# Performance work log

Hardware: AMD Instinct MI355X
Metric: run time of the kernel (lower is better)

The kernel has to match this reference:

```python
import jax, jax.numpy as jnp
import numpy as np
from jax import lax

BN_EPS = 1e-5


def _spatial_gate(x, w, g, b, m, v):
    # x: [N, C, H, W]; ChannelPool -> [N, 2, H, W]; 7x7 conv -> [N,1,H,W]; BN (eval); sigmoid gate
    comp = jnp.stack([jnp.max(x, axis=1), jnp.mean(x, axis=1)], axis=1)
    o = lax.conv_general_dilated(comp, w, (1, 1), [(3, 3), (3, 3)],
                                 dimension_numbers=('NCHW', 'OIHW', 'NCHW'))
    o = (o - m[None, :, None, None]) * lax.rsqrt(v + BN_EPS)[None, :, None, None] \
        * g[None, :, None, None] + b[None, :, None, None]
    s = jax.nn.sigmoid(o)
    return x * s


def _eca_sort(x, w_eca):
    # global avg pool -> sort channels desc -> 1D conv over sorted seq -> sigmoid -> unsort -> gate
    y = jnp.mean(x, axis=(2, 3))               # [N, C]
    order = jnp.argsort(-y, axis=1)            # descending sort indices
    rank = jnp.argsort(order, axis=1)          # inverse permutation
    ys = jnp.take_along_axis(y, order, axis=1)  # sorted descending
    k = w_eca.shape[-1]
    p = k // 2
    o = lax.conv_general_dilated(ys[:, None, :], w_eca, (1,), [(p, p)],
                                 dimension_numbers=('NCH', 'OIH', 'NCH'))[:, 0, :]
    sig = jax.nn.sigmoid(o)
    yr = jnp.take_along_axis(sig, rank, axis=1)  # reorder back per original index_select(rank)
    return x * yr[:, :, None, None]


def setup_inputs() -> dict:
    key = jax.random.key(0)
    ks = jax.random.split(key, 6)
    N, C, H, W = 32, 256, 56, 56
    inp = {
        'x': jax.random.normal(ks[0], (N, C, H, W), dtype=jnp.float32),
        'weight': jax.random.normal(ks[1], (1,), dtype=jnp.float32),
        'w_h': jax.random.normal(ks[2], (1, 2, 7, 7), dtype=jnp.float32) * 0.1,
        'g_h': jnp.ones((1,), jnp.float32), 'b_h': jnp.zeros((1,), jnp.float32),
        'm_h': jnp.zeros((1,), jnp.float32), 'v_h': jnp.ones((1,), jnp.float32),
        'w_w': jax.random.normal(ks[3], (1, 2, 7, 7), dtype=jnp.float32) * 0.1,
        'g_w': jnp.ones((1,), jnp.float32), 'b_w': jnp.zeros((1,), jnp.float32),
        'm_w': jnp.zeros((1,), jnp.float32), 'v_w': jnp.ones((1,), jnp.float32),
        'w_s': jax.random.normal(ks[4], (1, 2, 7, 7), dtype=jnp.float32) * 0.1,
        'g_s': jnp.ones((1,), jnp.float32), 'b_s': jnp.zeros((1,), jnp.float32),
        'm_s': jnp.zeros((1,), jnp.float32), 'v_s': jnp.ones((1,), jnp.float32),
        'w_eca': jax.random.normal(ks[5], (1, 1, 5), dtype=jnp.float32) * 0.3,
    }
    return inp


def reference(x, weight, w_h, g_h, b_h, m_h, v_h, w_w, g_w, b_w, m_w, v_w,
              w_s, g_s, b_s, m_s, v_s, w_eca):
    # branch 1: gate over H-as-channel (permute 0,2,1,3)
    xh = jnp.transpose(x, (0, 2, 1, 3))
    x11 = jnp.transpose(_spatial_gate(xh, w_h, g_h, b_h, m_h, v_h), (0, 2, 1, 3))
    # branch 2: gate over W-as-channel (permute 0,3,2,1)
    xw = jnp.transpose(x, (0, 3, 2, 1))
    x21 = jnp.transpose(_spatial_gate(xw, w_w, g_w, b_w, m_w, v_w), (0, 3, 2, 1))
    # branch 3: eca with sort/unsort
    x31 = _eca_sort(x, w_eca)
    # branch 4: plain spatial gate
    xo = _spatial_gate(x, w_s, g_s, b_s, m_s, v_s)
    return 0.23779 * xo + 0.24695 * x11 + 0.24365 * x21 + 0.27173 * x31
```

## Files before the change

### kernel.cpp

```cpp
#include <hip/hip_runtime.h>
#include <math.h>

#define N_ 32
#define C_ 256
#define H_ 56
#define W_ 56
#define HW_ (H_*W_)
#define HW4_ (HW_/4)
#define CHW_ (C_*HW_)
#define NHW_ (N_*HW_)
#define NHW4_ (NHW_/4)
#define NCW_ (N_*C_*W_)
#define NHC_ (N_*H_*C_)
#define BN_EPS_ 1e-5f

#define TLD 60
#define PLANES_PER_BLK 8
#define NB_PL 1024

#define SM_BUF1 3360
#define SM_CPMX 6720
#define SM_CPSM (6720 + 224)
#define SM_TOT  (6720 + 448)

#define F4MAX(a,b) do { (a).x=fmaxf((a).x,(b).x); (a).y=fmaxf((a).y,(b).y); \
                        (a).z=fmaxf((a).z,(b).z); (a).w=fmaxf((a).w,(b).w); } while(0)
#define F4ADD(a,b) do { (a).x+=(b).x; (a).y+=(b).y; (a).z+=(b).z; (a).w+=(b).w; } while(0)

__global__ __launch_bounds__(256, 4) void pools_k(
        const float* __restrict__ x,
        float* __restrict__ maxH, float* __restrict__ meanH,
        float* __restrict__ maxWt, float* __restrict__ meanWt,
        float* __restrict__ pmx, float* __restrict__ psm,
        float* __restrict__ y) {
    __shared__ float smem[SM_TOT];
    int b = blockIdx.x;
    int tid = threadIdx.x;
    const float4* x4 = (const float4*)x;
    float* buf0 = smem;
    float* buf1 = smem + SM_BUF1;
    float* cpmx = smem + SM_CPMX;
    float* cpsm = smem + SM_CPSM;
    int pb0 = b * PLANES_PER_BLK;
    float4 r0, r1, r2, r3;
    int row0 = tid / 14,          col0 = (tid % 14) * 4;
    int row1 = (tid + 256) / 14,  col1 = ((tid + 256) % 14) * 4;
    int row2 = (tid + 512) / 14,  col2 = ((tid + 512) % 14) * 4;
    int row3 = (tid + 768) / 14,  col3 = ((tid + 768) % 14) * 4;
    float4 amx0, amx1, amx2, amx3, asm0, asm1, asm2, asm3;
    amx0 = amx1 = amx2 = amx3 = make_float4(-INFINITY, -INFINITY, -INFINITY, -INFINITY);
    asm0 = asm1 = asm2 = asm3 = make_float4(0.f, 0.f, 0.f, 0.f);
    {
        size_t base = (size_t)pb0 * HW4_;
        r0 = x4[base + tid];
        r1 = x4[base + 256 + tid];
        r2 = x4[base + 512 + tid];
        if (tid < 16) r3 = x4[base + 768 + tid];
        F4MAX(amx0, r0); F4ADD(asm0, r0);
        F4MAX(amx1, r1); F4ADD(asm1, r1);
        F4MAX(amx2, r2); F4ADD(asm2, r2);
        if (tid < 16) { F4MAX(amx3, r3); F4ADD(asm3, r3); }
        *(float4*)&buf0[row0 * TLD + col0] = r0;
        *(float4*)&buf0[row1 * TLD + col1] = r1;
        *(float4*)&buf0[row2 * TLD + col2] = r2;
        if (tid < 16) *(float4*)&buf0[row3 * TLD + col3] = r3;
    }
    __syncthreads();
    for (int k = 0; k < PLANES_PER_BLK; ++k) {
        float* cur = (k & 1) ? buf1 : buf0;
        float* nxt = (k & 1) ? buf0 : buf1;
        int pb = pb0 + k;
        int n = pb >> 8, c = pb & 255;
        if (k < PLANES_PER_BLK - 1) {
            size_t base = (size_t)(pb + 1) * HW4_;
            r0 = x4[base + tid];
            r1 = x4[base + 256 + tid];
            r2 = x4[base + 512 + tid];
            if (tid < 16) r3 = x4[base + 768 + tid];
        }
        if (tid < 224) {
            int w = tid % 56, hq = tid / 56;
            const float* base = &cur[(hq * 14) * TLD + w];
            float mx = -INFINITY, sm = 0.f;
            #pragma unroll
            for (int hh = 0; hh < 14; ++hh) {
                float v = base[hh * TLD];
                mx = fmaxf(mx, v); sm += v;
            }
            cpmx[hq * 56 + w] = mx;
            cpsm[hq * 56 + w] = sm;
        }
        if (tid < 224) {
            int h = tid >> 2, kq = tid & 3;
            const float* base = &cur[h * TLD + kq * 14];
            float mx = -INFINITY, sm = 0.f;
            #pragma unroll
            for (int kk = 0; kk < 14; ++kk) {
                float v = base[kk];
                mx = fmaxf(mx, v); sm += v;
            }
            mx = fmaxf(mx, __shfl_xor(mx, 1)); sm += __shfl_xor(sm, 1);
            mx = fmaxf(mx, __shfl_xor(mx, 2)); sm += __shfl_xor(sm, 2);
            if (kq == 0) {
                int o = (n * C_ + c) * H_ + h;
                maxWt[o] = mx;
                meanWt[o] = sm * (1.f / W_);
            }
        }
        __syncthreads();
        float colsum = 0.f;
        if (tid < 56) {
            float mx = cpmx[tid], sm = cpsm[tid];
            #pragma unroll
            for (int j = 1; j < 4; ++j) {
                mx = fmaxf(mx, cpmx[j * 56 + tid]);
                sm += cpsm[j * 56 + tid];
            }
            int o = (n * C_ + c) * W_ + tid;
            maxH[o] = mx;
            meanH[o] = sm * (1.f / H_);
            colsum = sm;
        }
        if (tid < 64) {
            float t = colsum;
            #pragma unroll
            for (int off = 32; off >= 1; off >>= 1) t += __shfl_xor(t, off);
            if (tid == 0) y[n * C_ + c] = t * (1.f / HW_);
        }
        if (k < PLANES_PER_BLK - 1) {
            F4MAX(amx0, r0); F4ADD(asm0, r0);
            F4MAX(amx1, r1); F4ADD(asm1, r1);
            F4MAX(amx2, r2); F4ADD(asm2, r2);
            if (tid < 16) { F4MAX(amx3, r3); F4ADD(asm3, r3); }
            *(float4*)&nxt[row0 * TLD + col0] = r0;
            *(float4*)&nxt[row1 * TLD + col1] = r1;
            *(float4*)&nxt[row2 * TLD + col2] = r2;
            if (tid < 16) *(float4*)&nxt[row3 * TLD + col3] = r3;
        }
        __syncthreads();
    }
    {
        float4* PM = (float4*)pmx + (size_t)b * HW4_;
        float4* PS = (float4*)psm + (size_t)b * HW4_;
        PM[tid] = amx0;        PS[tid] = asm0;
        PM[tid + 256] = amx1;  PS[tid + 256] = asm1;
        PM[tid + 512] = amx2;  PS[tid + 512] = asm2;
        if (tid < 16) { PM[tid + 768] = amx3; PS[tid + 768] = asm3; }
    }
}

__global__ __launch_bounds__(256, 4) void cpool_final_k(
        const float* __restrict__ pmx, const float* __restrict__ psm,
        float* __restrict__ maxC, float* __restrict__ meanC) {
    __shared__ float4 smx[4][64];
    __shared__ float4 ssm[4][64];
    int bb = blockIdx.x;
    int tid = threadIdx.x;
    int oi = tid & 63, g4 = tid >> 6;
    int t = bb * 64 + oi;
    int n = t / HW4_, hw4 = t - n * HW4_;
    const float4* PM = (const float4*)pmx + (size_t)(n * 32 + g4 * 8) * HW4_ + hw4;
    const float4* PS = (const float4*)psm + (size_t)(n * 32 + g4 * 8) * HW4_ + hw4;
    float4 mx = make_float4(-INFINITY, -INFINITY, -INFINITY, -INFINITY);
    float4 sm = make_float4(0.f, 0.f, 0.f, 0.f);
    #pragma unroll
    for (int g = 0; g < 8; ++g) {
        float4 v = PM[(size_t)g * HW4_];
        float4 s = PS[(size_t)g * HW4_];
        F4MAX(mx, v);
        F4ADD(sm, s);
    }
    smx[g4][oi] = mx;
    ssm[g4][oi] = sm;
    __syncthreads();
    if (tid < 64) {
        float4 m = smx[0][tid];
        #pragma unroll
        for (int j = 1; j < 4; ++j) {
            float4 v = smx[j][tid];
            F4MAX(m, v);
        }
        ((float4*)maxC)[bb * 64 + tid] = m;
    } else if (tid < 128) {
        int t2 = tid - 64;
        float4 s = ssm[0][t2];
        #pragma unroll
        for (int j = 1; j < 4; ++j) {
            float4 v = ssm[j][t2];
            F4ADD(s, v);
        }
        s.x *= (1.f / C_); s.y *= (1.f / C_); s.z *= (1.f / C_); s.w *= (1.f / C_);
        ((float4*)meanC)[bb * 64 + t2] = s;
    }
}

template <int R, int Cc, bool TR>
__device__ __forceinline__ void conv7_part(int t, const float* __restrict__ p0,
                                           const float* __restrict__ p1,
                                           const float* __restrict__ wt,
                                           float g, float bb, float m, float v,
                                           float* __restrict__ out) {
    const int per = R * Cc;
    int n = t / per;
    int r2 = t - n * per;
    int i = r2 / Cc, j = r2 - i * Cc;
    const float* b0 = p0 + (size_t)n * per;
    const float* b1 = p1 + (size_t)n * per;
    float acc = 0.f;
    #pragma unroll
    for (int ki = 0; ki < 7; ++ki) {
        int ii = i + ki - 3;
        if (ii < 0 || ii >= R) continue;
        #pragma unroll
        for (int kj = 0; kj < 7; ++kj) {
            int jj = j + kj - 3;
            if (jj < 0 || jj >= Cc) continue;
            int idx = ii * Cc + jj;
            int wi = TR ? (kj * 7 + ki) : (ki * 7 + kj);
            acc += b0[idx] * wt[wi] + b1[idx] * wt[49 + wi];
        }
    }
    float o = (acc - m) * rsqrtf(v + BN_EPS_) * g + bb;
    out[t] = 1.f / (1.f + expf(-o));
}

#define NB_SS (NHW_ / 256)
#define NB_SH (NCW_ / 256)
#define NB_SW (NHC_ / 256)

__global__ __launch_bounds__(256) void conv_eca_k(
        const float* __restrict__ maxC, const float* __restrict__ meanC,
        const float* __restrict__ maxH, const float* __restrict__ meanH,
        const float* __restrict__ maxWt, const float* __restrict__ meanWt,
        const float* __restrict__ w_s, const float* __restrict__ g_s,
        const float* __restrict__ b_s, const float* __restrict__ m_s,
        const float* __restrict__ v_s,
        const float* __restrict__ w_h, const float* __restrict__ g_h,
        const float* __restrict__ b_h, const float* __restrict__ m_h,
        const float* __restrict__ v_h,
        const float* __restrict__ w_w, const float* __restrict__ g_w,
        const float* __restrict__ b_w, const float* __restrict__ m_w,
        const float* __restrict__ v_w,
        const float* __restrict__ y, const float* __restrict__ w_eca,
        float* __restrict__ s_s, float* __restrict__ s_h, float* __restrict__ s_wt,
        float* __restrict__ gate) {
    __shared__ float sv[C_];
    __shared__ int si[C_];
    int b = blockIdx.x;
    int tid = threadIdx.x;
    if (b < NB_SS) {
        conv7_part<H_, W_, false>(b * 256 + tid, maxC, meanC, w_s, g_s[0], b_s[0],
                                  m_s[0], v_s[0], s_s);
    } else if (b < NB_SS + NB_SH) {
        conv7_part<C_, W_, false>((b - NB_SS) * 256 + tid, maxH, meanH, w_h, g_h[0],
                                  b_h[0], m_h[0], v_h[0], s_h);
    } else if (b < NB_SS + NB_SH + NB_SW) {
        conv7_part<C_, H_, true>((b - NB_SS - NB_SH) * 256 + tid, maxWt, meanWt, w_w,
                                 g_w[0], b_w[0], m_w[0], v_w[0], s_wt);
    } else {
        int n = b - (NB_SS + NB_SH + NB_SW);
        sv[tid] = y[n * C_ + tid];
        si[tid] = tid;
        __syncthreads();
        for (int k = 2; k <= C_; k <<= 1) {
            for (int j = k >> 1; j > 0; j >>= 1) {
                int ixj = tid ^ j;
                if (ixj > tid) {
                    float v1 = sv[tid], v2 = sv[ixj];
                    int i1 = si[tid], i2 = si[ixj];
                    bool before = (v1 > v2) || (v1 == v2 && i1 < i2);
                    bool dir = ((tid & k) == 0);
                    if (dir ? !before : before) {
                        sv[tid] = v2; sv[ixj] = v1;
                        si[tid] = i2; si[ixj] = i1;
                    }
                }
                __syncthreads();
            }
        }
        float o = 0.f;
        #pragma unroll
        for (int j = 0; j < 5; ++j) {
            int p = tid + j - 2;
            if (p >= 0 && p < C_) o += sv[p] * w_eca[j];
        }
        gate[n * C_ + si[tid]] = 1.f / (1.f + expf(-o));
    }
}

__global__ __launch_bounds__(256) void apply_k(
        const float* __restrict__ x, const float* __restrict__ s_s,
        const float* __restrict__ s_h, const float* __restrict__ s_wt,
        const float* __restrict__ gate, float* __restrict__ out) {
    int t0 = blockIdx.x * 512 + threadIdx.x;
    #pragma unroll
    for (int r = 0; r < 2; ++r) {
        int t = t0 + r * 256;
        int f = t * 4;
        int n = f / CHW_;
        int rem = f - n * CHW_;
        int c = rem / HW_;
        int hw = rem - c * HW_;
        int h = hw / W_;
        int w = hw - h * W_;
        float4 xv = ((const float4*)x)[t];
        float4 s4 = *(const float4*)(s_s + (size_t)n * HW_ + hw);
        float4 h4 = *(const float4*)(s_h + ((size_t)n * C_ + c) * W_ + w);
        float sw = s_wt[((size_t)n * C_ + c) * H_ + h];
        float ge = gate[n * C_ + c];
        float base = 0.24365f * sw + 0.27173f * ge;
        float4 o;
        o.x = xv.x * (0.23779f * s4.x + 0.24695f * h4.x + base);
        o.y = xv.y * (0.23779f * s4.y + 0.24695f * h4.y + base);
        o.z = xv.z * (0.23779f * s4.z + 0.24695f * h4.z + base);
        o.w = xv.w * (0.23779f * s4.w + 0.24695f * h4.w + base);
        ((float4*)out)[t] = o;
    }
}

extern "C" void kernel_launch(void* const* d_in, const int* in_sizes, int n_in,
                              void* d_out, int out_size, void* d_ws, size_t ws_size,
                              hipStream_t stream) {
    const float* x     = (const float*)d_in[0];
    const float* w_h   = (const float*)d_in[2];
    const float* g_h   = (const float*)d_in[3];
    const float* b_h   = (const float*)d_in[4];
    const float* m_h   = (const float*)d_in[5];
    const float* v_h   = (const float*)d_in[6];
    const float* w_w   = (const float*)d_in[7];
    const float* g_w   = (const float*)d_in[8];
    const float* b_w   = (const float*)d_in[9];
    const float* m_w   = (const float*)d_in[10];
    const float* v_w   = (const float*)d_in[11];
    const float* w_s   = (const float*)d_in[12];
    const float* g_s   = (const float*)d_in[13];
    const float* b_s   = (const float*)d_in[14];
    const float* m_s   = (const float*)d_in[15];
    const float* v_s   = (const float*)d_in[16];
    const float* w_eca = (const float*)d_in[17];
    float* out = (float*)d_out;

    float* ws    = (float*)d_ws;
    float* maxC  = ws;
    float* meanC = maxC  + NHW_;
    float* maxH  = meanC + NHW_;
    float* meanH = maxH  + NCW_;
    float* maxWt = meanH + NCW_;
    float* meanWt= maxWt + NHC_;
    float* s_s   = meanWt+ NHC_;
    float* s_h   = s_s   + NHW_;
    float* s_wt  = s_h   + NCW_;
    float* yv    = s_wt  + NHC_;
    float* gate  = yv    + N_ * C_;
    float* pmx   = gate  + N_ * C_;
    float* psm   = pmx   + (size_t)NB_PL * HW_;

    pools_k<<<NB_PL, 256, 0, stream>>>(x, maxH, meanH, maxWt, meanWt, pmx, psm, yv);

    cpool_final_k<<<NHW4_ / 64, 256, 0, stream>>>(pmx, psm, maxC, meanC);

    int conv_blocks = NB_SS + NB_SH + NB_SW + N_;
    conv_eca_k<<<conv_blocks, 256, 0, stream>>>(maxC, meanC, maxH, meanH, maxWt, meanWt,
                                                w_s, g_s, b_s, m_s, v_s,
                                                w_h, g_h, b_h, m_h, v_h,
                                                w_w, g_w, b_w, m_w, v_w,
                                                yv, w_eca, s_s, s_h, s_wt, gate);

    apply_k<<<(N_ * CHW_ / 4) / 512, 256, 0, stream>>>(x, s_s, s_h, s_wt, gate, out);
}
```

Before: 93.70 us.

## Deepen pools kernel prefetch to two planes with triple-buffered LDS

The pooling kernel now processes 16 planes per block instead of 8 and keeps two planes of global loads in flight using two register sets and three LDS tile buffers. The loop is unrolled by two so one plane's loads are issued while the previous plane is reduced. This aims to hide more global memory latency and to halve the partial channel-pool buffers that the final reduction kernel reads. In exchange it uses more registers and shared memory per block and launches half as many blocks, which may lower occupancy and parallelism.

```diff
diff --git a/kernel.cpp b/kernel.cpp
--- a/kernel.cpp
+++ b/kernel.cpp
@@ -15,13 +15,13 @@
 #define BN_EPS_ 1e-5f
 
 #define TLD 60
-#define PLANES_PER_BLK 8
-#define NB_PL 1024
-
-#define SM_BUF1 3360
-#define SM_CPMX 6720
-#define SM_CPSM (6720 + 224)
-#define SM_TOT  (6720 + 448)
+#define PPB 16
+#define NB_PL 512
+
+#define SM_B(i) ((i) * 3360)
+#define SM_CPMX 10080
+#define SM_CPSM (10080 + 224)
+#define SM_TOT  (10080 + 448)
 
 #define F4MAX(a,b) do { (a).x=fmaxf((a).x,(b).x); (a).y=fmaxf((a).y,(b).y); \
                         (a).z=fmaxf((a).z,(b).z); (a).w=fmaxf((a).w,(b).w); } while(0)
@@ -37,108 +37,108 @@
     int b = blockIdx.x;
     int tid = threadIdx.x;
     const float4* x4 = (const float4*)x;
-    float* buf0 = smem;
-    float* buf1 = smem + SM_BUF1;
     float* cpmx = smem + SM_CPMX;
     float* cpsm = smem + SM_CPSM;
-    int pb0 = b * PLANES_PER_BLK;
-    float4 r0, r1, r2, r3;
+    int pb0 = b * PPB;
     int row0 = tid / 14,          col0 = (tid % 14) * 4;
     int row1 = (tid + 256) / 14,  col1 = ((tid + 256) % 14) * 4;
     int row2 = (tid + 512) / 14,  col2 = ((tid + 512) % 14) * 4;
     int row3 = (tid + 768) / 14,  col3 = ((tid + 768) % 14) * 4;
+    float4 a0, a1, a2, a3;
+    float4 b0_, b1_, b2_, b3_;
     float4 amx0, amx1, amx2, amx3, asm0, asm1, asm2, asm3;
     amx0 = amx1 = amx2 = amx3 = make_float4(-INFINITY, -INFINITY, -INFINITY, -INFINITY);
     asm0 = asm1 = asm2 = asm3 = make_float4(0.f, 0.f, 0.f, 0.f);
-    {
-        size_t base = (size_t)pb0 * HW4_;
-        r0 = x4[base + tid];
-        r1 = x4[base + 256 + tid];
-        r2 = x4[base + 512 + tid];
-        if (tid < 16) r3 = x4[base + 768 + tid];
-        F4MAX(amx0, r0); F4ADD(asm0, r0);
-        F4MAX(amx1, r1); F4ADD(asm1, r1);
-        F4MAX(amx2, r2); F4ADD(asm2, r2);
-        if (tid < 16) { F4MAX(amx3, r3); F4ADD(asm3, r3); }
-        *(float4*)&buf0[row0 * TLD + col0] = r0;
-        *(float4*)&buf0[row1 * TLD + col1] = r1;
-        *(float4*)&buf0[row2 * TLD + col2] = r2;
-        if (tid < 16) *(float4*)&buf0[row3 * TLD + col3] = r3;
-    }
+
+#define ISSUE(R0,R1,R2,R3, P) { size_t _ba = (size_t)(pb0 + (P)) * HW4_;          \
+        R0 = x4[_ba + tid]; R1 = x4[_ba + 256 + tid]; R2 = x4[_ba + 512 + tid];   \
+        if (tid < 16) R3 = x4[_ba + 768 + tid]; }
+#define FOLD(R0,R1,R2,R3) { F4MAX(amx0,R0); F4ADD(asm0,R0);                       \
+        F4MAX(amx1,R1); F4ADD(asm1,R1); F4MAX(amx2,R2); F4ADD(asm2,R2);           \
+        if (tid < 16) { F4MAX(amx3,R3); F4ADD(asm3,R3); } }
+#define STAGE(BUF, R0,R1,R2,R3) { float* _d = smem + (BUF);                       \
+        *(float4*)&_d[row0*TLD+col0] = R0; *(float4*)&_d[row1*TLD+col1] = R1;     \
+        *(float4*)&_d[row2*TLD+col2] = R2;                                        \
+        if (tid < 16) *(float4*)&_d[row3*TLD+col3] = R3; }
+
+    ISSUE(a0, a1, a2, a3, 0);
+    FOLD(a0, a1, a2, a3);
+    STAGE(SM_B(0), a0, a1, a2, a3);
+    ISSUE(b0_, b1_, b2_, b3_, 1);
     __syncthreads();
-    for (int k = 0; k < PLANES_PER_BLK; ++k) {
-        float* cur = (k & 1) ? buf1 : buf0;
-        float* nxt = (k & 1) ? buf0 : buf1;
-        int pb = pb0 + k;
-        int n = pb >> 8, c = pb & 255;
-        if (k < PLANES_PER_BLK - 1) {
-            size_t base = (size_t)(pb + 1) * HW4_;
-            r0 = x4[base + tid];
-            r1 = x4[base + 256 + tid];
-            r2 = x4[base + 512 + tid];
-            if (tid < 16) r3 = x4[base + 768 + tid];
-        }
-        if (tid < 224) {
-            int w = tid % 56, hq = tid / 56;
-            const float* base = &cur[(hq * 14) * TLD + w];
-            float mx = -INFINITY, sm = 0.f;
-            #pragma unroll
-            for (int hh = 0; hh < 14; ++hh) {
-                float v = base[hh * TLD];
-                mx = fmaxf(mx, v); sm += v;
-            }
-            cpmx[hq * 56 + w] = mx;
-            cpsm[hq * 56 + w] = sm;
-        }
-        if (tid < 224) {
-            int h = tid >> 2, kq = tid & 3;
-            const float* base = &cur[h * TLD + kq * 14];
-            float mx = -INFINITY, sm = 0.f;
-            #pragma unroll
-            for (int kk = 0; kk < 14; ++kk) {
-                float v = base[kk];
-                mx = fmaxf(mx, v); sm += v;
-            }
-            mx = fmaxf(mx, __shfl_xor(mx, 1)); sm += __shfl_xor(sm, 1);
-            mx = fmaxf(mx, __shfl_xor(mx, 2)); sm += __shfl_xor(sm, 2);
-            if (kq == 0) {
-                int o = (n * C_ + c) * H_ + h;
-                maxWt[o] = mx;
-                meanWt[o] = sm * (1.f / W_);
-            }
+
+#define COMPUTE(K) {                                                              \
+        const float* cur = smem + SM_B((K) % 3);                                  \
+        int pb = pb0 + (K);                                                       \
+        int n = pb >> 8, c = pb & 255;                                            \
+        if (tid < 224) {                     \
+            int w = tid % 56, hq = tid / 56;                                      \
+            const float* base = &cur[(hq * 14) * TLD + w];                        \
+            float mx = -INFINITY, sm = 0.f;                                       \
+            _Pragma("unroll")                                                     \
+            for (int hh = 0; hh < 14; ++hh) {                                     \
+                float v = base[hh * TLD];                                         \
+                mx = fmaxf(mx, v); sm += v;                                       \
+            }                                                                     \
+            cpmx[hq * 56 + w] = mx; cpsm[hq * 56 + w] = sm;                       \
+        }                                                                         \
+        if (tid < 224) {                     \
+            int h = tid >> 2, kq = tid & 3;                                       \
+            const float* base = &cur[h * TLD + kq * 14];                          \
+            float mx = -INFINITY, sm = 0.f;                                       \
+            _Pragma("unroll")                                                     \
+            for (int kk = 0; kk < 14; ++kk) {                                     \
+                float v = base[kk];                                               \
+                mx = fmaxf(mx, v); sm += v;                                       \
+            }                                                                     \
+            mx = fmaxf(mx, __shfl_xor(mx, 1)); sm += __shfl_xor(sm, 1);           \
+            mx = fmaxf(mx, __shfl_xor(mx, 2)); sm += __shfl_xor(sm, 2);           \
+            if (kq == 0) {                                                        \
+                int o = (n * C_ + c) * H_ + h;                                    \
+                maxWt[o] = mx; meanWt[o] = sm * (1.f / W_);                       \
+            }                                                                     \
+        }                                                                         \
+        __syncthreads();                                                          \
+        float colsum = 0.f;                                                       \
+        if (tid < 56) {                                                           \
+            float mx = cpmx[tid], sm = cpsm[tid];                                 \
+            _Pragma("unroll")                                                     \
+            for (int j = 1; j < 4; ++j) {                                         \
+                mx = fmaxf(mx, cpmx[j * 56 + tid]);                               \
+                sm += cpsm[j * 56 + tid];                                         \
+            }                                                                     \
+            int o = (n * C_ + c) * W_ + tid;                                      \
+            maxH[o] = mx; meanH[o] = sm * (1.f / H_);                             \
+            colsum = sm;                                                          \
+        }                                                                         \
+        if (tid < 64) {                                                           \
+            float t = colsum;                                                     \
+            _Pragma("unroll")                                                     \
+            for (int off = 32; off >= 1; off >>= 1) t += __shfl_xor(t, off);      \
+            if (tid == 0) y[n * C_ + c] = t * (1.f / HW_);                        \
+        }                                                                         \
+    }
+
+    #pragma unroll
+    for (int k2 = 0; k2 < PPB / 2; ++k2) {
+        const int k = 2 * k2;
+        if (k + 2 < PPB) ISSUE(a0, a1, a2, a3, k + 2);
+        COMPUTE(k);
+        FOLD(b0_, b1_, b2_, b3_);
+        STAGE(SM_B((k + 1) % 3), b0_, b1_, b2_, b3_);
+        __syncthreads();
+        if (k + 3 < PPB) ISSUE(b0_, b1_, b2_, b3_, k + 3);
+        COMPUTE(k + 1);
+        if (k + 2 < PPB) {
+            FOLD(a0, a1, a2, a3);
+            STAGE(SM_B((k + 2) % 3), a0, a1, a2, a3);
         }
         __syncthreads();
-        float colsum = 0.f;
-        if (tid < 56) {
-            float mx = cpmx[tid], sm = cpsm[tid];
-            #pragma unroll
-            for (int j = 1; j < 4; ++j) {
-                mx = fmaxf(mx, cpmx[j * 56 + tid]);
-                sm += cpsm[j * 56 + tid];
-            }
-            int o = (n * C_ + c) * W_ + tid;
-            maxH[o] = mx;
-            meanH[o] = sm * (1.f / H_);
-            colsum = sm;
-        }
-        if (tid < 64) {
-            float t = colsum;
-            #pragma unroll
-            for (int off = 32; off >= 1; off >>= 1) t += __shfl_xor(t, off);
-            if (tid == 0) y[n * C_ + c] = t * (1.f / HW_);
-        }
-        if (k < PLANES_PER_BLK - 1) {
-            F4MAX(amx0, r0); F4ADD(asm0, r0);
-            F4MAX(amx1, r1); F4ADD(asm1, r1);
-            F4MAX(amx2, r2); F4ADD(asm2, r2);
-            if (tid < 16) { F4MAX(amx3, r3); F4ADD(asm3, r3); }
-            *(float4*)&nxt[row0 * TLD + col0] = r0;
-            *(float4*)&nxt[row1 * TLD + col1] = r1;
-            *(float4*)&nxt[row2 * TLD + col2] = r2;
-            if (tid < 16) *(float4*)&nxt[row3 * TLD + col3] = r3;
-        }
-        __syncthreads();
-    }
+    }
+#undef ISSUE
+#undef FOLD
+#undef STAGE
+#undef COMPUTE
     {
         float4* PM = (float4*)pmx + (size_t)b * HW4_;
         float4* PS = (float4*)psm + (size_t)b * HW4_;
@@ -159,12 +159,12 @@
     int oi = tid & 63, g4 = tid >> 6;
     int t = bb * 64 + oi;
     int n = t / HW4_, hw4 = t - n * HW4_;
-    const float4* PM = (const float4*)pmx + (size_t)(n * 32 + g4 * 8) * HW4_ + hw4;
-    const float4* PS = (const float4*)psm + (size_t)(n * 32 + g4 * 8) * HW4_ + hw4;
+    const float4* PM = (const float4*)pmx + (size_t)(n * 16 + g4 * 4) * HW4_ + hw4;
+    const float4* PS = (const float4*)psm + (size_t)(n * 16 + g4 * 4) * HW4_ + hw4;
     float4 mx = make_float4(-INFINITY, -INFINITY, -INFINITY, -INFINITY);
     float4 sm = make_float4(0.f, 0.f, 0.f, 0.f);
     #pragma unroll
-    for (int g = 0; g < 8; ++g) {
+    for (int g = 0; g < 4; ++g) {
         float4 v = PM[(size_t)g * HW4_];
         float4 s = PS[(size_t)g * HW4_];
         F4MAX(mx, v);
@@ -176,19 +176,13 @@
     if (tid < 64) {
         float4 m = smx[0][tid];
         #pragma unroll
-        for (int j = 1; j < 4; ++j) {
-            float4 v = smx[j][tid];
-            F4MAX(m, v);
-        }
+        for (int j = 1; j < 4; ++j) F4MAX(m, smx[j][tid]);
         ((float4*)maxC)[bb * 64 + tid] = m;
     } else if (tid < 128) {
         int t2 = tid - 64;
         float4 s = ssm[0][t2];
         #pragma unroll
-        for (int j = 1; j < 4; ++j) {
-            float4 v = ssm[j][t2];
-            F4ADD(s, v);
-        }
+        for (int j = 1; j < 4; ++j) F4ADD(s, ssm[j][t2]);
         s.x *= (1.f / C_); s.y *= (1.f / C_); s.z *= (1.f / C_); s.w *= (1.f / C_);
         ((float4*)meanC)[bb * 64 + t2] = s;
     }
```

Result: no change. 92.35 us (median of 2 runs) (-1.4%).
